# Performance work log

Measured on AMD Instinct MI355X. Metric: run time of the kernel, lower is better.

Reference implementation:

```python
import jax, jax.numpy as jnp
import numpy as np

N_NODES = 4096        # number of sum nodes in this layer
N_CHILD = 16384       # total number of child-layer nodes
DEGREE = 64           # fan-in per sum node
NNZ = N_NODES * DEGREE
BATCH = 128


def setup_inputs() -> dict:
    key = jax.random.key(0)
    k1, k2, k3 = jax.random.split(key, 3)
    child_ll = jax.random.normal(k1, (BATCH, N_CHILD), dtype=jnp.float32)
    log_w = jax.random.normal(k2, (NNZ,), dtype=jnp.float32)
    # each sum node has exactly DEGREE incoming edges (sorted segment ids)
    rows = jnp.repeat(jnp.arange(N_NODES, dtype=jnp.int32), DEGREE)
    cols = jax.random.randint(k3, (NNZ,), 0, N_CHILD, dtype=jnp.int32)
    return {"child_ll": child_ll, "log_w": log_w, "rows": rows, "cols": cols}


def _segment_logsumexp(v, seg, num_segments):
    # v: [E, ...], seg: [E] -> [num_segments, ...], numerically stable
    m = jax.ops.segment_max(v, seg, num_segments=num_segments)
    m = jax.lax.stop_gradient(m)
    s = jax.ops.segment_sum(jnp.exp(v - m[seg]), seg, num_segments=num_segments)
    return m + jnp.log(s)


def reference(child_ll, log_w, rows, cols):
    # per-edge weighted child log-likelihood: [E, B]
    v = child_ll.T[cols] + log_w[:, None]
    # unnormalized sum-node log-likelihood: [N, B]
    ll = _segment_logsumexp(v, rows, N_NODES)
    # per-node log normalization constant logsumexp(log_w) over each row: [N]
    log_z = _segment_logsumexp(log_w, rows, N_NODES)
    return (ll - log_z[:, None]).T  # [B, N]
```

## Files before the change

kernel.cpp:

```cpp
#include <hip/hip_runtime.h>
#include <hip/hip_bf16.h>

#define N_NODES 4096
#define N_CHILD 16384
#define DEGREE  64
#define BATCH   128
#define NN      8

__global__ __launch_bounds__(256)
void exp_transpose_kernel(const float* __restrict__ in,
                          __hip_bfloat16* __restrict__ out) {
    __shared__ float tile[32][33];
    const int c0 = blockIdx.x * 32;
    const int b0 = blockIdx.y * 32;
    const int tx = threadIdx.x;
    const int ty = threadIdx.y;
#pragma unroll
    for (int j = 0; j < 32; j += 8)
        tile[ty + j][tx] = __expf(in[(size_t)(b0 + ty + j) * N_CHILD + (c0 + tx)]);
    __syncthreads();
#pragma unroll
    for (int j = 0; j < 32; j += 8)
        out[(size_t)(c0 + ty + j) * BATCH + (b0 + tx)] =
            __float2bfloat16(tile[tx][ty + j]);
}

__global__ __launch_bounds__(1024, 8)
void sum_layer_kernel(const __hip_bfloat16* __restrict__ childE,
                      const float* __restrict__ log_w,
                      const int*   __restrict__ cols,
                      float* __restrict__ out)
{
    const int tid  = threadIdx.x;
    const int wv   = __builtin_amdgcn_readfirstlane(tid >> 6);
    const int j    = wv >> 1;
    const int h    = wv & 1;
    const int lane = tid & 63;
    const int n0   = blockIdx.x * NN;
    const int e0   = (n0 + j) * DEGREE + h * 32;

    __shared__ float2 part[NN][2][65];
    __shared__ float  swp[NN][2];

    const float ew = __expf(log_w[e0 + (lane & 31)]);
    float sw = ew;
#pragma unroll
    for (int off = 16; off >= 1; off >>= 1)
        sw += __shfl_xor(sw, off);
    if (lane == 0) swp[j][h] = sw;

    const unsigned int* __restrict__ rowE = (const unsigned int*)childE;

    float s0a = 0.f, s0b = 0.f, s1a = 0.f, s1b = 0.f;
#pragma unroll
    for (int d = 0; d < 32; d += 2) {
        const int ca = cols[e0 + d];
        const int cb = cols[e0 + d + 1];
        const float ewa = __shfl(ew, d);
        const float ewb = __shfl(ew, d + 1);
        const unsigned int ua = rowE[ca * 64 + lane];
        const unsigned int ub = rowE[cb * 64 + lane];
        s0a = fmaf(__uint_as_float(ua << 16),          ewa, s0a);
        s1a = fmaf(__uint_as_float(ua & 0xffff0000u),  ewa, s1a);
        s0b = fmaf(__uint_as_float(ub << 16),          ewb, s0b);
        s1b = fmaf(__uint_as_float(ub & 0xffff0000u),  ewb, s1b);
    }
    part[j][h][lane] = make_float2(s0a + s0b, s1a + s1b);

    __syncthreads();

    {
        const int jo = tid & (NN - 1);
        const int b  = tid >> 3;
        const float2 p0 = part[jo][0][b >> 1];
        const float2 p1 = part[jo][1][b >> 1];
        const float s = (b & 1) ? (p0.y + p1.y) : (p0.x + p1.x);
        const float lz = __logf(swp[jo][0] + swp[jo][1]);
        out[(size_t)b * N_NODES + n0 + jo] = __logf(s) - lz;
    }
}

extern "C" void kernel_launch(void* const* d_in, const int* in_sizes, int n_in,
                              void* d_out, int out_size, void* d_ws, size_t ws_size,
                              hipStream_t stream) {
    const float* child_ll = (const float*)d_in[0];
    const float* log_w    = (const float*)d_in[1];
    const int*   cols     = (const int*)d_in[3];
    float*       out      = (float*)d_out;

    __hip_bfloat16* childE = (__hip_bfloat16*)d_ws;

    {
        dim3 tb(32, 8), tg(N_CHILD / 32, BATCH / 32);
        exp_transpose_kernel<<<tg, tb, 0, stream>>>(child_ll, childE);
    }

    sum_layer_kernel<<<N_NODES / NN, 1024, 0, stream>>>(childE, log_w, cols, out);
}
```

Measured before the change: 73.85 us.

## Assign one node per wave with 16-byte gathers and LDS-staged edge metadata

Restructures the sum-layer kernel so each wave handles a full node (64 edges). Each lane gathers a uint4 holding 8 bf16 batch values instead of 4-byte loads, and the precomputed edge weight and byte offset are staged in LDS. Partial sums are reduced with cross-lane shuffles and the results go through LDS so the output stores are coalesced. This cuts the number of memory instructions and removes the per-edge scalar cols loads, at the cost of more registers (launch bounds drop to 4 waves per SIMD) and an extra barrier.

```diff
diff --git a/kernel.cpp b/kernel.cpp
--- a/kernel.cpp
+++ b/kernel.cpp
@@ -5,7 +5,7 @@
 #define N_CHILD 16384
 #define DEGREE  64
 #define BATCH   128
-#define NN      8
+#define NWAVE   16
 
 __global__ __launch_bounds__(256)
 void exp_transpose_kernel(const float* __restrict__ in,
@@ -25,59 +25,72 @@
             __float2bfloat16(tile[tx][ty + j]);
 }
 
-__global__ __launch_bounds__(1024, 8)
+__global__ __launch_bounds__(1024, 4)
 void sum_layer_kernel(const __hip_bfloat16* __restrict__ childE,
                       const float* __restrict__ log_w,
                       const int*   __restrict__ cols,
                       float* __restrict__ out)
 {
     const int tid  = threadIdx.x;
-    const int wv   = __builtin_amdgcn_readfirstlane(tid >> 6);
-    const int j    = wv >> 1;
-    const int h    = wv & 1;
+    const int w    = __builtin_amdgcn_readfirstlane(tid >> 6);
     const int lane = tid & 63;
-    const int n0   = blockIdx.x * NN;
-    const int e0   = (n0 + j) * DEGREE + h * 32;
+    const int node = blockIdx.x * NWAVE + w;
+    const int e0   = node * DEGREE;
 
-    __shared__ float2 part[NN][2][65];
-    __shared__ float  swp[NN][2];
+    __shared__ float2 meta[NWAVE][DEGREE];
+    __shared__ float  res[NWAVE][BATCH + 2];
 
-    const float ew = __expf(log_w[e0 + (lane & 31)]);
+    const float ew  = __expf(log_w[e0 + lane]);
+    const int   col = cols[e0 + lane];
+    meta[w][lane] = make_float2(ew, __int_as_float(col << 8));
+
     float sw = ew;
 #pragma unroll
-    for (int off = 16; off >= 1; off >>= 1)
-        sw += __shfl_xor(sw, off);
-    if (lane == 0) swp[j][h] = sw;
-
-    const unsigned int* __restrict__ rowE = (const unsigned int*)childE;
-
-    float s0a = 0.f, s0b = 0.f, s1a = 0.f, s1b = 0.f;
-#pragma unroll
-    for (int d = 0; d < 32; d += 2) {
-        const int ca = cols[e0 + d];
-        const int cb = cols[e0 + d + 1];
-        const float ewa = __shfl(ew, d);
-        const float ewb = __shfl(ew, d + 1);
-        const unsigned int ua = rowE[ca * 64 + lane];
-        const unsigned int ub = rowE[cb * 64 + lane];
-        s0a = fmaf(__uint_as_float(ua << 16),          ewa, s0a);
-        s1a = fmaf(__uint_as_float(ua & 0xffff0000u),  ewa, s1a);
-        s0b = fmaf(__uint_as_float(ub << 16),          ewb, s0b);
-        s1b = fmaf(__uint_as_float(ub & 0xffff0000u),  ewb, s1b);
-    }
-    part[j][h][lane] = make_float2(s0a + s0b, s1a + s1b);
+    for (int off = 32; off >= 1; off >>= 1) sw += __shfl_xor(sw, off);
+    const float lz = __logf(sw);
 
     __syncthreads();
 
+    const int g   = lane >> 4;
+    const int m16 = (lane & 15) * 16;
+
+    float acc[8] = {0.f, 0.f, 0.f, 0.f, 0.f, 0.f, 0.f, 0.f};
+
+#pragma unroll
+    for (int it = 0; it < DEGREE / 4; ++it) {
+        const float2   md  = meta[w][it * 4 + g];
+        const unsigned off = __float_as_uint(md.y) + m16;
+        const uint4    u   = *(const uint4*)((const char*)childE + off);
+        const float    ewv = md.x;
+        acc[0] = fmaf(__uint_as_float(u.x << 16),         ewv, acc[0]);
+        acc[1] = fmaf(__uint_as_float(u.x & 0xffff0000u), ewv, acc[1]);
+        acc[2] = fmaf(__uint_as_float(u.y << 16),         ewv, acc[2]);
+        acc[3] = fmaf(__uint_as_float(u.y & 0xffff0000u), ewv, acc[3]);
+        acc[4] = fmaf(__uint_as_float(u.z << 16),         ewv, acc[4]);
+        acc[5] = fmaf(__uint_as_float(u.z & 0xffff0000u), ewv, acc[5]);
+        acc[6] = fmaf(__uint_as_float(u.w << 16),         ewv, acc[6]);
+        acc[7] = fmaf(__uint_as_float(u.w & 0xffff0000u), ewv, acc[7]);
+    }
+
+#pragma unroll
+    for (int j = 0; j < 8; ++j) {
+        acc[j] += __shfl_xor(acc[j], 16);
+        acc[j] += __shfl_xor(acc[j], 32);
+    }
+
     {
-        const int jo = tid & (NN - 1);
-        const int b  = tid >> 3;
-        const float2 p0 = part[jo][0][b >> 1];
-        const float2 p1 = part[jo][1][b >> 1];
-        const float s = (b & 1) ? (p0.y + p1.y) : (p0.x + p1.x);
-        const float lz = __logf(swp[jo][0] + swp[jo][1]);
-        out[(size_t)b * N_NODES + n0 + jo] = __logf(s) - lz;
+        const int b = (lane & 15) * 8 + 2 * g;
+        float2 r = make_float2(__logf(acc[2 * g])     - lz,
+                               __logf(acc[2 * g + 1]) - lz);
+        *(float2*)&res[w][b] = r;
     }
+    __syncthreads();
+
+    const int w2 = tid & 15;
+    const int b0 = tid >> 4;
+    const int n0 = blockIdx.x * NWAVE;
+    out[(size_t)b0        * N_NODES + n0 + w2] = res[w2][b0];
+    out[(size_t)(b0 + 64) * N_NODES + n0 + w2] = res[w2][b0 + 64];
 }
 
 extern "C" void kernel_launch(void* const* d_in, const int* in_sizes, int n_in,
@@ -95,5 +108,5 @@
         exp_transpose_kernel<<<tg, tb, 0, stream>>>(child_ll, childE);
     }
 
-    sum_layer_kernel<<<N_NODES / NN, 1024, 0, stream>>>(childE, log_w, cols, out);
+    sum_layer_kernel<<<N_NODES / NWAVE, 1024, 0, stream>>>(childE, log_w, cols, out);
 }
```

After: 73.66 us. Within noise of the previous version (-0.3%).
